# Kernel optimization log

Measured on AMD Instinct MI355X. Metric: run time of the kernel, lower is better.

## Reference

```python
import jax, jax.numpy as jnp
import numpy as np

HIDDEN_DIM = 1024
NUM_HEADS = 16
HEAD_DIM = HIDDEN_DIM // NUM_HEADS


def setup_inputs() -> dict:
    key = jax.random.key(0)
    ks = jax.random.split(key, 9)
    s = 1.0 / np.sqrt(HIDDEN_DIM)
    x = jax.random.normal(ks[0], (2, 2048, HIDDEN_DIM), dtype=jnp.float32)
    Wq = jax.random.uniform(ks[1], (HIDDEN_DIM, HIDDEN_DIM), jnp.float32, -s, s)
    bq = jax.random.uniform(ks[2], (HIDDEN_DIM,), jnp.float32, -s, s)
    Wk = jax.random.uniform(ks[3], (HIDDEN_DIM, HIDDEN_DIM), jnp.float32, -s, s)
    bk = jax.random.uniform(ks[4], (HIDDEN_DIM,), jnp.float32, -s, s)
    Wv = jax.random.uniform(ks[5], (HIDDEN_DIM, HIDDEN_DIM), jnp.float32, -s, s)
    bv = jax.random.uniform(ks[6], (HIDDEN_DIM,), jnp.float32, -s, s)
    Wo = jax.random.uniform(ks[7], (HIDDEN_DIM, HIDDEN_DIM), jnp.float32, -s, s)
    bo = jax.random.uniform(ks[8], (HIDDEN_DIM,), jnp.float32, -s, s)
    return {"x": x, "Wq": Wq, "bq": bq, "Wk": Wk, "bk": bk,
            "Wv": Wv, "bv": bv, "Wo": Wo, "bo": bo}


def reference(x, Wq, bq, Wk, bk, Wv, bv, Wo, bo):
    B, M, D = x.shape
    H, Dh = NUM_HEADS, HEAD_DIM
    # projections -> [B, H, M, Dh]
    def split_heads(t):
        return t.reshape(B, M, H, Dh).transpose(0, 2, 1, 3)
    q = split_heads(x @ Wq.T + bq)
    k = split_heads(x @ Wk.T + bk)
    v = split_heads(x @ Wv.T + bv)
    scores = jnp.einsum('bhmd,bhnd->bhmn', q, k) / np.sqrt(Dh).astype(np.float32)
    # multiplicative diagonal-zero mask: zero the diagonal of the score matrix
    diag_zero = 1.0 - jnp.eye(M, dtype=scores.dtype)  # [M, M]
    scores = scores * diag_zero
    attn = jax.nn.softmax(scores, axis=-1)
    context = jnp.einsum('bhmn,bhnd->bhmd', attn, v)
    context = context.transpose(0, 2, 1, 3).reshape(B, M, D)
    return context @ Wo.T + bo
```

## Files before the change

### kernel.cpp

```cpp
#include <hip/hip_runtime.h>
#include <stdint.h>

typedef _Float16 f16;
typedef __attribute__((ext_vector_type(8))) _Float16 f16x8;
typedef __attribute__((ext_vector_type(4))) _Float16 f16x4;
typedef __attribute__((ext_vector_type(2))) __fp16 fp16x2;
typedef __attribute__((ext_vector_type(4))) float f32x4;

#define HD 1024
#define NH 16
#define DH 64
#define BB 2
#define MM 2048
#define BH (BB*NH)
#define MT (BB*MM)

__device__ __forceinline__ void gl_lds16(const f16* g, f16* l) {
    __builtin_amdgcn_global_load_lds((const __attribute__((address_space(1))) uint32_t*)g,
                                     (__attribute__((address_space(3))) uint32_t*)l, 16, 0, 0);
}

__device__ __forceinline__ float fexp2(float x) {
    float r; asm("v_exp_f32 %0, %1" : "=v"(r) : "v"(x)); return r;
}

__global__ void cvt_all(const float* __restrict__ x,  const float* __restrict__ wq,
                        const float* __restrict__ wk, const float* __restrict__ wv,
                        const float* __restrict__ wo, f16* __restrict__ dst) {
    const int XN4 = MT * HD / 4;
    const int WN4 = HD * HD / 4;
    int i = blockIdx.x * blockDim.x + threadIdx.x;
    if (i >= XN4 + 4 * WN4) return;
    const float* s; int off;
    if (i < XN4) { s = x; off = i; }
    else {
        int k = i - XN4, wsel = k >> 18;
        off = k & (WN4 - 1);
        s = wsel == 0 ? wq : wsel == 1 ? wk : wsel == 2 ? wv : wo;
    }
    float4 v = ((const float4*)s)[off];
    f16x4 h;
    h[0] = (f16)v.x; h[1] = (f16)v.y; h[2] = (f16)v.z; h[3] = (f16)v.w;
    ((f16x4*)dst)[i] = h;
}

template<int MODE>
__global__ __launch_bounds__(256, 3) void gemm_m97(const f16* __restrict__ A,
                                                   const f16* __restrict__ W,
                                                   const float* __restrict__ b0,
                                                   const float* __restrict__ b1,
                                                   const float* __restrict__ b2,
                                                   f16* __restrict__ oh,
                                                   float* __restrict__ of) {
    __shared__ f16 As[128 * 32];
    __shared__ f16 Bs[128 * 32];
    const int bid = blockIdx.x;
    int bn, bm;
    if (MODE == 0) { int xcd = bid & 7, r = bid >> 3; bn = xcd * 3 + (r >> 5); bm = r & 31; }
    else           { bn = bid & 7; bm = bid >> 3; }
    const int t = threadIdx.x, w = t >> 6, lane = t & 63;
    const int wr = w >> 1, wc = w & 1, lr = lane & 15, lg = lane >> 4;
    f32x4 acc[4][4] = {};

    const int srow = w * 16 + (lane >> 2);
    const int schunk = lane & 3;
    const f16* Ab = A + (size_t)(bm * 128) * HD;
    const f16* Wb = W + (size_t)(bn * 128) * HD;
    f16* Asw = As + w * 512;
    f16* Bsw = Bs + w * 512;

    #pragma unroll
    for (int i = 0; i < 2; i++) {
        int r = i * 64 + srow;
        int gc = ((schunk ^ ((r >> 1) & 3)) * 8);
        gl_lds16(Ab + (size_t)r * HD + gc, Asw + i * 2048);
        gl_lds16(Wb + (size_t)r * HD + gc, Bsw + i * 2048);
    }

    for (int k0 = 0;;) {
        __syncthreads();
        f16x8 af[4], bf[4];
        #pragma unroll
        for (int i = 0; i < 4; i++) {
            int ra = wr * 64 + i * 16 + lr;
            af[i] = *(const f16x8*)(As + ra * 32 + ((lg ^ ((ra >> 1) & 3)) * 8));
            int rb = wc * 64 + i * 16 + lr;
            bf[i] = *(const f16x8*)(Bs + rb * 32 + ((lg ^ ((rb >> 1) & 3)) * 8));
        }
        #pragma unroll
        for (int i = 0; i < 4; i++)
            #pragma unroll
            for (int j = 0; j < 4; j++)
                acc[i][j] = __builtin_amdgcn_mfma_f32_16x16x32_f16(af[i], bf[j], acc[i][j], 0, 0, 0);
        k0 += 32;
        if (k0 >= HD) break;
        __syncthreads();
        #pragma unroll
        for (int i = 0; i < 2; i++) {
            int r = i * 64 + srow;
            int gc = ((schunk ^ ((r >> 1) & 3)) * 8);
            gl_lds16(Ab + (size_t)r * HD + k0 + gc, Asw + i * 2048);
            gl_lds16(Wb + (size_t)r * HD + k0 + gc, Bsw + i * 2048);
        }
    }

    if (MODE == 0) {
        const int mat = bn >> 3;
        const float* bp = mat == 0 ? b0 : mat == 1 ? b1 : b2;
        f16* base = oh + (size_t)mat * BH * MM * DH;
        #pragma unroll
        for (int i = 0; i < 4; i++) {
            #pragma unroll
            for (int j = 0; j < 4; j++) {
                int n = bn * 128 + wc * 64 + j * 16 + lr;
                int nn = n & 1023, h = nn >> 6, dh = nn & 63;
                float bvv = bp[nn];
                int mg0 = bm * 128 + wr * 64 + i * 16 + lg * 4;
                int b = mg0 >> 11, mmr0 = mg0 & 2047;
                if (mat == 2) {
                    f16x4 o;
                    #pragma unroll
                    for (int r = 0; r < 4; r++) o[r] = (f16)(acc[i][j][r] + bvv);
                    *(f16x4*)(base + ((size_t)((b * NH + h) * DH + dh)) * MM + mmr0) = o;
                } else {
                    float sc = (mat == 0) ? 0.1803368801111204f : 1.0f;
                    #pragma unroll
                    for (int r = 0; r < 4; r++)
                        base[((size_t)((b * NH + h) * MM + mmr0 + r)) * DH + dh] =
                            (f16)((acc[i][j][r] + bvv) * sc);
                }
            }
        }
    } else {
        #pragma unroll
        for (int i = 0; i < 4; i++)
            #pragma unroll
            for (int j = 0; j < 4; j++) {
                int n = bn * 128 + wc * 64 + j * 16 + lr;
                float bvv = b0[n];
                #pragma unroll
                for (int r = 0; r < 4; r++) {
                    int mg = bm * 128 + wr * 64 + i * 16 + lg * 4 + r;
                    of[(size_t)mg * HD + n] = acc[i][j][r] + bvv;
                }
            }
    }
}

__global__ __launch_bounds__(512, 4) void attn_kernel(const f16* __restrict__ Q,
                                                      const f16* __restrict__ K,
                                                      const f16* __restrict__ Vt,
                                                      f16* __restrict__ ctx) {
    __shared__ f16 Kl[3][64][64];
    __shared__ f16 Vl[3][64][64];
    __shared__ f16 Pl[8][32][32];
    const int bid = blockIdx.x;
    const int xcd = bid & 7, idx = bid >> 3;
    const int bh = xcd * 4 + (idx >> 4);
    const int qblk2 = idx & 15;

    const int t = threadIdx.x, w = t >> 6, lane = t & 63;
    const int lr = lane & 15, lg = lane >> 4;
    const int wq = w >> 1, wkv = w & 1;
    const int q0B = qblk2 * 128 + wq * 32;
    const int kvb = wkv * 32;
    const int dtile = q0B >> 6;
    const bool dwave = (wkv == (wq & 1));

    const f16* Qb = Q + (size_t)bh * MM * DH;
    const f16* Kb = K + (size_t)bh * MM * DH;
    const f16* Vb = Vt + (size_t)bh * DH * MM;

    const int srowS = lane >> 3;
    const int sxc = ((lane & 7) ^ srowS) * 8;
    const int lds_r = w * 8;

    f16x8 qfr[2][2];
    #pragma unroll
    for (int qf = 0; qf < 2; qf++)
        #pragma unroll
        for (int c = 0; c < 2; c++)
            qfr[qf][c] = *(const f16x8*)(Qb + (size_t)(q0B + qf * 16 + lr) * DH + c * 32 + lg * 8);

    f32x4 po[4][2] = {};
    float lsum0 = 0.f, lsum1 = 0.f;
    const int sw = (lr & 7) * 8;
    const int ko0 = (lg * 8) ^ sw, ko1 = (32 + lg * 8) ^ sw;
    const int vko = (kvb + lg * 8) ^ sw;
    const int ps = (lr >> 1) & 3;
    f16* Pw = &Pl[w][0][0];
    const int pro = lr * 32 + ((lg ^ ps) * 8);

    #pragma unroll
    for (int tt = 0; tt < 2; tt++) {
        int row = lds_r + srowS;
        gl_lds16(Kb + (size_t)(tt * 64 + row) * DH + sxc, &Kl[tt][lds_r][0]);
        gl_lds16(Vb + (size_t)row * MM + tt * 64 + sxc, &Vl[tt][lds_r][0]);
    }

#define ATTN_BODY(CUR, NXT, IT, VMN)                                                         \
    {                                                                                        \
        const int it_ = (IT);                                                                \
        asm volatile("s_waitcnt vmcnt(" #VMN ")" ::: "memory");    \
        __builtin_amdgcn_s_barrier();                                  \
        if (it_ < 30) {        \
            const int jn = (it_ + 2) * 64;                                                   \
            int row = lds_r + srowS;                                                         \
            gl_lds16(Kb + (size_t)(jn + row) * DH + sxc, &Kl[NXT][lds_r][0]);                \
            gl_lds16(Vb + (size_t)row * MM + jn + sxc, &Vl[NXT][lds_r][0]);                  \
        }                                                                                    \
        f32x4 s00 = {}, s01 = {}, s10 = {}, s11 = {};                         \
        __builtin_amdgcn_s_setprio(1);                                                       \
        {                                                                                    \
            const f16* kr0 = &Kl[CUR][kvb + lr][0];                                          \
            f16x8 ka = *(const f16x8*)(kr0 + ko0);                                           \
            f16x8 kb = *(const f16x8*)(kr0 + ko1);                                           \
            s00 = __builtin_amdgcn_mfma_f32_16x16x32_f16(ka, qfr[0][0], s00, 0, 0, 0);       \
            s00 = __builtin_amdgcn_mfma_f32_16x16x32_f16(kb, qfr[0][1], s00, 0, 0, 0);       \
            s01 = __builtin_amdgcn_mfma_f32_16x16x32_f16(ka, qfr[1][0], s01, 0, 0, 0);       \
            s01 = __builtin_amdgcn_mfma_f32_16x16x32_f16(kb, qfr[1][1], s01, 0, 0, 0);       \
            const f16* kr1 = &Kl[CUR][kvb + 16 + lr][0];                                     \
            f16x8 kc = *(const f16x8*)(kr1 + ko0);                                           \
            f16x8 kd = *(const f16x8*)(kr1 + ko1);                                           \
            s10 = __builtin_amdgcn_mfma_f32_16x16x32_f16(kc, qfr[0][0], s10, 0, 0, 0);       \
            s10 = __builtin_amdgcn_mfma_f32_16x16x32_f16(kd, qfr[0][1], s10, 0, 0, 0);       \
            s11 = __builtin_amdgcn_mfma_f32_16x16x32_f16(kc, qfr[1][0], s11, 0, 0, 0);       \
            s11 = __builtin_amdgcn_mfma_f32_16x16x32_f16(kd, qfr[1][1], s11, 0, 0, 0);       \
        }                                                                                    \
        __builtin_amdgcn_s_setprio(0);                                                       \
        if (it_ == dtile && dwave) {         \
            int rr = lr - lg * 4;                                                            \
            if (rr >= 0 && rr < 4) { s00[rr] = 0.f; s11[rr] = 0.f; }                         \
        }                                                                                    \
        _Pragma("unroll")                                                                    \
        for (int u = 0; u < 4; u++) {                                                        \
            const f32x4 sv = (u == 0) ? s00 : (u == 1) ? s01 : (u == 2) ? s10 : s11;         \
            const int fq = u >> 1, qf = u & 1;                                               \
            float p0 = fexp2(sv[0]), p1 = fexp2(sv[1]);                                      \
            float p2 = fexp2(sv[2]), p3 = fexp2(sv[3]);                                      \
            if (qf == 0) lsum0 += (p0 + p1) + (p2 + p3);                                     \
            else         lsum1 += (p0 + p1) + (p2 + p3);                                     \
            fp16x2 lo = __builtin_amdgcn_cvt_pkrtz(p0, p1);                                  \
            fp16x2 hi = __builtin_amdgcn_cvt_pkrtz(p2, p3);                                  \
            uint2 pr; pr.x = __builtin_bit_cast(uint32_t, lo);                               \
            pr.y = __builtin_bit_cast(uint32_t, hi);                                         \
            *(f16x4*)(Pw + (qf * 16 + lr) * 32 +                                             \
                      (((fq * 2 + (lg >> 1)) ^ ps) * 8) + (lg & 1) * 4) =                    \
                __builtin_bit_cast(f16x4, pr);                                               \
        }                                                                                    \
        asm volatile("s_waitcnt lgkmcnt(0)" ::: "memory");      \
        f16x8 pf0 = *(const f16x8*)(Pw + pro);                                               \
        f16x8 pf1 = *(const f16x8*)(Pw + 512 + pro);                                         \
        __builtin_amdgcn_s_setprio(1);                                                       \
        _Pragma("unroll")                                                                    \
        for (int df = 0; df < 4; df++) {                                                     \
            const f16* vr = &Vl[CUR][df * 16 + lr][0];                                       \
            f16x8 va = *(const f16x8*)(vr + vko);                                            \
            po[df][0] = __builtin_amdgcn_mfma_f32_16x16x32_f16(va, pf0, po[df][0], 0, 0, 0); \
            po[df][1] = __builtin_amdgcn_mfma_f32_16x16x32_f16(va, pf1, po[df][1], 0, 0, 0); \
        }                                                                                    \
        __builtin_amdgcn_s_setprio(0);                                                       \
    }

    for (int itp = 0; itp < 10; ++itp) {
        ATTN_BODY(0, 2, 3 * itp,     2)
        ATTN_BODY(1, 0, 3 * itp + 1, 2)
        ATTN_BODY(2, 1, 3 * itp + 2, 2)
    }
    ATTN_BODY(0, 2, 30, 2)
    ATTN_BODY(1, 0, 31, 0)
#undef ATTN_BODY

    lsum0 += __shfl_xor(lsum0, 16); lsum0 += __shfl_xor(lsum0, 32);
    lsum1 += __shfl_xor(lsum1, 16); lsum1 += __shfl_xor(lsum1, 32);
    __syncthreads();
    float* shf0 = (float*)(&Kl[0][0][0]);
    float* shf1 = (float*)(&Vl[0][0][0]);
    float* shl  = (float*)(&Pl[0][0][0]);
    const int xi = wq * 64 + lane;
    if (wkv == 1) {
        float* d0 = shf0 + (size_t)xi * 17;
        float* d1 = shf1 + (size_t)xi * 17;
        #pragma unroll
        for (int df = 0; df < 4; df++) {
            *(f32x4*)(d0 + df * 4) = po[df][0];
            *(f32x4*)(d1 + df * 4) = po[df][1];
        }
        shl[xi * 2]     = lsum0;
        shl[xi * 2 + 1] = lsum1;
    }
    __syncthreads();
    if (wkv == 0) {
        const float* s0 = shf0 + (size_t)xi * 17;
        const float* s1 = shf1 + (size_t)xi * 17;
        const float inv0 = 1.f / (lsum0 + shl[xi * 2]);
        const float inv1 = 1.f / (lsum1 + shl[xi * 2 + 1]);
        const int b = bh >> 4, hh = bh & 15;
        #pragma unroll
        for (int qf = 0; qf < 2; qf++) {
            const float inv = qf ? inv1 : inv0;
            const float* s = qf ? s1 : s0;
            f16* cp = ctx + ((size_t)(b * MM + q0B + qf * 16 + lr)) * HD + hh * DH;
            #pragma unroll
            for (int df = 0; df < 4; df++) {
                f16x4 o;
                #pragma unroll
                for (int r = 0; r < 4; r++)
                    o[r] = (f16)((po[df][qf][r] + s[df * 4 + r]) * inv);
                *(f16x4*)(cp + df * 16 + lg * 4) = o;
            }
        }
    }
}

extern "C" void kernel_launch(void* const* d_in, const int* in_sizes, int n_in,
                              void* d_out, int out_size, void* d_ws, size_t ws_size,
                              hipStream_t stream) {
    const float* x  = (const float*)d_in[0];
    const float* Wq = (const float*)d_in[1];
    const float* bq = (const float*)d_in[2];
    const float* Wk = (const float*)d_in[3];
    const float* bk = (const float*)d_in[4];
    const float* Wv = (const float*)d_in[5];
    const float* bv = (const float*)d_in[6];
    const float* Wo = (const float*)d_in[7];
    const float* bo = (const float*)d_in[8];
    float* out = (float*)d_out;

    f16* xh  = (f16*)d_ws;
    f16* wqh = xh  + (size_t)MT * HD;
    f16* woh = wqh + (size_t)3 * HD * HD;
    f16* Qh  = woh + (size_t)HD * HD;
    f16* ctxh= Qh  + (size_t)3 * BH * MM * DH;

    const int total4 = MT * HD / 4 + HD * HD;
    cvt_all<<<(total4 + 255) / 256, 256, 0, stream>>>(x, Wq, Wk, Wv, Wo, xh);

    gemm_m97<0><<<768, 256, 0, stream>>>(xh, wqh, bq, bk, bv, Qh, nullptr);

    attn_kernel<<<512, 512, 0, stream>>>(Qh, Qh + (size_t)BH * MM * DH,
                                         Qh + (size_t)2 * BH * MM * DH, ctxh);

    gemm_m97<1><<<256, 256, 0, stream>>>(ctxh, woh, bo, nullptr, nullptr, nullptr, out);
}
```

Measured before the change: 115.6 us.

## Triple-buffer GEMM LDS tiles with two-stage-ahead async global loads

Replaces the single-buffer load/compute loop in the projection GEMM with a three-slot LDS ring, issuing global-to-LDS loads two K-steps ahead and waiting with explicit vmcnt counts plus one barrier per step. The goal is to hide global memory latency behind MFMA work and remove one of the two barriers per iteration. LDS use per block triples to 48KB, which may lower occupancy against the launch bound of 3 blocks, and correctness depends on the hand-set vmcnt values.

```diff
diff --git a/kernel.cpp b/kernel.cpp
--- a/kernel.cpp
+++ b/kernel.cpp
@@ -52,8 +52,8 @@
                                                    const float* __restrict__ b2,
                                                    f16* __restrict__ oh,
                                                    float* __restrict__ of) {
-    __shared__ f16 As[128 * 32];
-    __shared__ f16 Bs[128 * 32];
+    __shared__ f16 As[3][128 * 32];
+    __shared__ f16 Bs[3][128 * 32];
     const int bid = blockIdx.x;
     int bn, bm;
     if (MODE == 0) { int xcd = bid & 7, r = bid >> 3; bn = xcd * 3 + (r >> 5); bm = r & 31; }
@@ -66,43 +66,47 @@
     const int schunk = lane & 3;
     const f16* Ab = A + (size_t)(bm * 128) * HD;
     const f16* Wb = W + (size_t)(bn * 128) * HD;
-    f16* Asw = As + w * 512;
-    f16* Bsw = Bs + w * 512;
-
-    #pragma unroll
-    for (int i = 0; i < 2; i++) {
-        int r = i * 64 + srow;
-        int gc = ((schunk ^ ((r >> 1) & 3)) * 8);
-        gl_lds16(Ab + (size_t)r * HD + gc, Asw + i * 2048);
-        gl_lds16(Wb + (size_t)r * HD + gc, Bsw + i * 2048);
-    }
-
-    for (int k0 = 0;;) {
-        __syncthreads();
-        f16x8 af[4], bf[4];
-        #pragma unroll
-        for (int i = 0; i < 4; i++) {
-            int ra = wr * 64 + i * 16 + lr;
-            af[i] = *(const f16x8*)(As + ra * 32 + ((lg ^ ((ra >> 1) & 3)) * 8));
-            int rb = wc * 64 + i * 16 + lr;
-            bf[i] = *(const f16x8*)(Bs + rb * 32 + ((lg ^ ((rb >> 1) & 3)) * 8));
-        }
-        #pragma unroll
-        for (int i = 0; i < 4; i++)
-            #pragma unroll
-            for (int j = 0; j < 4; j++)
-                acc[i][j] = __builtin_amdgcn_mfma_f32_16x16x32_f16(af[i], bf[j], acc[i][j], 0, 0, 0);
-        k0 += 32;
-        if (k0 >= HD) break;
-        __syncthreads();
-        #pragma unroll
-        for (int i = 0; i < 2; i++) {
-            int r = i * 64 + srow;
-            int gc = ((schunk ^ ((r >> 1) & 3)) * 8);
-            gl_lds16(Ab + (size_t)r * HD + k0 + gc, Asw + i * 2048);
-            gl_lds16(Wb + (size_t)r * HD + k0 + gc, Bsw + i * 2048);
-        }
-    }
+
+#define GSTAGE(BUF, K0)                                                         \
+    _Pragma("unroll")                                                           \
+    for (int i = 0; i < 2; i++) {                                               \
+        int r = i * 64 + srow;                                                  \
+        int gc = ((schunk ^ ((r >> 1) & 3)) * 8);                               \
+        gl_lds16(Ab + (size_t)r * HD + (K0) + gc, &As[BUF][w * 512 + i * 2048]);\
+        gl_lds16(Wb + (size_t)r * HD + (K0) + gc, &Bs[BUF][w * 512 + i * 2048]);\
+    }
+
+#define GSTEP(CUR, STG, T, VMN)                                                 \
+    {                                                                           \
+        asm volatile("s_waitcnt vmcnt(" #VMN ")" ::: "memory");                 \
+        __builtin_amdgcn_s_barrier();                                           \
+        if ((T) + 2 < 32) { GSTAGE(STG, ((T) + 2) * 32) }                       \
+        f16x8 af[4], bf[4];                                                     \
+        _Pragma("unroll")                                                       \
+        for (int i = 0; i < 4; i++) {                                           \
+            int ra = wr * 64 + i * 16 + lr;                                     \
+            af[i] = *(const f16x8*)(&As[CUR][ra * 32 + ((lg ^ ((ra >> 1) & 3)) * 8)]); \
+            int rb = wc * 64 + i * 16 + lr;                                     \
+            bf[i] = *(const f16x8*)(&Bs[CUR][rb * 32 + ((lg ^ ((rb >> 1) & 3)) * 8)]); \
+        }                                                                       \
+        _Pragma("unroll")                                                       \
+        for (int i = 0; i < 4; i++)                                             \
+            _Pragma("unroll")                                                   \
+            for (int j = 0; j < 4; j++)                                         \
+                acc[i][j] = __builtin_amdgcn_mfma_f32_16x16x32_f16(af[i], bf[j], acc[i][j], 0, 0, 0); \
+    }
+
+    GSTAGE(0, 0)
+    GSTAGE(1, 32)
+    for (int itp = 0; itp < 10; ++itp) {
+        GSTEP(0, 2, 3 * itp,     4)
+        GSTEP(1, 0, 3 * itp + 1, 4)
+        GSTEP(2, 1, 3 * itp + 2, 4)
+    }
+    GSTEP(0, 2, 30, 4)
+    GSTEP(1, 0, 31, 0)
+#undef GSTAGE
+#undef GSTEP
 
     if (MODE == 0) {
         const int mat = bn >> 3;
```

Result: no change. 117.0 us (+1.2%).

## Software-pipeline attention loop: defer PV MFMA one iteration with double-buffered P

Applied to the files above, without the earlier changes.

Restructures the attention main loop so that each iteration first runs the P·V MFMAs for the previous KV tile, then computes QK^T and the exp for the current tile. P gets a double buffer in LDS, and V loads are staged one tile ahead instead of two. The aim is to remove the lgkmcnt(0) stall between writing P and reading it back, so the LDS round-trip latency overlaps with the next tile's QK MFMAs. It costs twice the LDS for P, which may affect occupancy, and needs an epilogue for the final PV.

```diff
diff --git a/kernel.cpp b/kernel.cpp
--- a/kernel.cpp
+++ b/kernel.cpp
@@ -153,7 +153,7 @@
                                                       f16* __restrict__ ctx) {
     __shared__ f16 Kl[3][64][64];
     __shared__ f16 Vl[3][64][64];
-    __shared__ f16 Pl[8][32][32];
+    __shared__ f16 Pl[8][2][32][32];
     const int bid = blockIdx.x;
     const int xcd = bid & 7, idx = bid >> 3;
     const int bh = xcd * 4 + (idx >> 4);
@@ -188,38 +188,54 @@
     const int ko0 = (lg * 8) ^ sw, ko1 = (32 + lg * 8) ^ sw;
     const int vko = (kvb + lg * 8) ^ sw;
     const int ps = (lr >> 1) & 3;
-    f16* Pw = &Pl[w][0][0];
     const int pro = lr * 32 + ((lg ^ ps) * 8);
 
-    #pragma unroll
-    for (int tt = 0; tt < 2; tt++) {
+    {
         int row = lds_r + srowS;
-        gl_lds16(Kb + (size_t)(tt * 64 + row) * DH + sxc, &Kl[tt][lds_r][0]);
-        gl_lds16(Vb + (size_t)row * MM + tt * 64 + sxc, &Vl[tt][lds_r][0]);
-    }
-
-#define ATTN_BODY(CUR, NXT, IT, VMN)                                                         \
+        gl_lds16(Kb + (size_t)row * DH + sxc, &Kl[0][lds_r][0]);
+        gl_lds16(Kb + (size_t)(64 + row) * DH + sxc, &Kl[1][lds_r][0]);
+        gl_lds16(Vb + (size_t)row * MM + sxc, &Vl[0][lds_r][0]);
+    }
+
+#define ABODY(KC, VP, VS, PW, PR, IT, VMN, DOPV)                                             \
     {                                                                                        \
         const int it_ = (IT);                                                                \
-        asm volatile("s_waitcnt vmcnt(" #VMN ")" ::: "memory");    \
-        __builtin_amdgcn_s_barrier();                                  \
-        if (it_ < 30) {        \
-            const int jn = (it_ + 2) * 64;                                                   \
+        asm volatile("s_waitcnt vmcnt(" #VMN ")" ::: "memory");      \
+        __builtin_amdgcn_s_barrier();                                                        \
+        if (it_ + 2 <= 31) {                                                                 \
             int row = lds_r + srowS;                                                         \
-            gl_lds16(Kb + (size_t)(jn + row) * DH + sxc, &Kl[NXT][lds_r][0]);                \
-            gl_lds16(Vb + (size_t)row * MM + jn + sxc, &Vl[NXT][lds_r][0]);                  \
+            gl_lds16(Kb + (size_t)((it_ + 2) * 64 + row) * DH + sxc,                         \
+                     &Kl[(KC + 2) % 3][lds_r][0]);                                           \
+        }                                                                                    \
+        if (it_ + 1 <= 31) {                                                                 \
+            int row = lds_r + srowS;                                                         \
+            gl_lds16(Vb + (size_t)row * MM + (it_ + 1) * 64 + sxc, &Vl[VS][lds_r][0]);       \
+        }                                                                                    \
+        if (DOPV) {        \
+            const f16* Pr = &Pl[w][PR][0][0];                                                \
+            f16x8 pf0 = *(const f16x8*)(Pr + pro);                                           \
+            f16x8 pf1 = *(const f16x8*)(Pr + 512 + pro);                                     \
+            __builtin_amdgcn_s_setprio(1);                                                   \
+            _Pragma("unroll")                                                                \
+            for (int df = 0; df < 4; df++) {                                                 \
+                const f16* vr = &Vl[VP][df * 16 + lr][0];                                    \
+                f16x8 va = *(const f16x8*)(vr + vko);                                        \
+                po[df][0] = __builtin_amdgcn_mfma_f32_16x16x32_f16(va, pf0, po[df][0], 0, 0, 0); \
+                po[df][1] = __builtin_amdgcn_mfma_f32_16x16x32_f16(va, pf1, po[df][1], 0, 0, 0); \
+            }                                                                                \
+            __builtin_amdgcn_s_setprio(0);                                                   \
         }                                                                                    \
         f32x4 s00 = {}, s01 = {}, s10 = {}, s11 = {};                         \
         __builtin_amdgcn_s_setprio(1);                                                       \
         {                                                                                    \
-            const f16* kr0 = &Kl[CUR][kvb + lr][0];                                          \
+            const f16* kr0 = &Kl[KC][kvb + lr][0];                                           \
             f16x8 ka = *(const f16x8*)(kr0 + ko0);                                           \
             f16x8 kb = *(const f16x8*)(kr0 + ko1);                                           \
             s00 = __builtin_amdgcn_mfma_f32_16x16x32_f16(ka, qfr[0][0], s00, 0, 0, 0);       \
             s00 = __builtin_amdgcn_mfma_f32_16x16x32_f16(kb, qfr[0][1], s00, 0, 0, 0);       \
             s01 = __builtin_amdgcn_mfma_f32_16x16x32_f16(ka, qfr[1][0], s01, 0, 0, 0);       \
             s01 = __builtin_amdgcn_mfma_f32_16x16x32_f16(kb, qfr[1][1], s01, 0, 0, 0);       \
-            const f16* kr1 = &Kl[CUR][kvb + 16 + lr][0];                                     \
+            const f16* kr1 = &Kl[KC][kvb + 16 + lr][0];                                      \
             f16x8 kc = *(const f16x8*)(kr1 + ko0);                                           \
             f16x8 kd = *(const f16x8*)(kr1 + ko1);                                           \
             s10 = __builtin_amdgcn_mfma_f32_16x16x32_f16(kc, qfr[0][0], s10, 0, 0, 0);       \
@@ -232,6 +248,7 @@
             int rr = lr - lg * 4;                                                            \
             if (rr >= 0 && rr < 4) { s00[rr] = 0.f; s11[rr] = 0.f; }                         \
         }                                                                                    \
+        f16* Pwr = &Pl[w][PW][0][0];                                                         \
         _Pragma("unroll")                                                                    \
         for (int u = 0; u < 4; u++) {                                                        \
             const f32x4 sv = (u == 0) ? s00 : (u == 1) ? s01 : (u == 2) ? s10 : s11;         \
@@ -244,39 +261,46 @@
             fp16x2 hi = __builtin_amdgcn_cvt_pkrtz(p2, p3);                                  \
             uint2 pr; pr.x = __builtin_bit_cast(uint32_t, lo);                               \
             pr.y = __builtin_bit_cast(uint32_t, hi);                                         \
-            *(f16x4*)(Pw + (qf * 16 + lr) * 32 +                                             \
+            *(f16x4*)(Pwr + (qf * 16 + lr) * 32 +                                            \
                       (((fq * 2 + (lg >> 1)) ^ ps) * 8) + (lg & 1) * 4) =                    \
                 __builtin_bit_cast(f16x4, pr);                                               \
         }                                                                                    \
-        asm volatile("s_waitcnt lgkmcnt(0)" ::: "memory");      \
-        f16x8 pf0 = *(const f16x8*)(Pw + pro);                                               \
-        f16x8 pf1 = *(const f16x8*)(Pw + 512 + pro);                                         \
-        __builtin_amdgcn_s_setprio(1);                                                       \
-        _Pragma("unroll")                                                                    \
-        for (int df = 0; df < 4; df++) {                                                     \
-            const f16* vr = &Vl[CUR][df * 16 + lr][0];                                       \
-            f16x8 va = *(const f16x8*)(vr + vko);                                            \
-            po[df][0] = __builtin_amdgcn_mfma_f32_16x16x32_f16(va, pf0, po[df][0], 0, 0, 0); \
-            po[df][1] = __builtin_amdgcn_mfma_f32_16x16x32_f16(va, pf1, po[df][1], 0, 0, 0); \
-        }                                                                                    \
-        __builtin_amdgcn_s_setprio(0);                                                       \
-    }
-
-    for (int itp = 0; itp < 10; ++itp) {
-        ATTN_BODY(0, 2, 3 * itp,     2)
-        ATTN_BODY(1, 0, 3 * itp + 1, 2)
-        ATTN_BODY(2, 1, 3 * itp + 2, 2)
-    }
-    ATTN_BODY(0, 2, 30, 2)
-    ATTN_BODY(1, 0, 31, 0)
-#undef ATTN_BODY
+    }
+
+    ABODY(0, 2, 1, 0, 1, 0, 2, 0)
+    for (int itp = 0; itp < 5; ++itp) {
+        const int s0 = 6 * itp;
+        ABODY(1, 0, 2, 1, 0, s0 + 1, 2, 1)
+        ABODY(2, 1, 0, 0, 1, s0 + 2, 2, 1)
+        ABODY(0, 2, 1, 1, 0, s0 + 3, 2, 1)
+        ABODY(1, 0, 2, 0, 1, s0 + 4, 2, 1)
+        ABODY(2, 1, 0, 1, 0, s0 + 5, 2, 1)
+        ABODY(0, 2, 1, 0, 1, s0 + 6, 2, 1)
+    }
+    ABODY(1, 0, 2, 1, 0, 31, 1, 1)
+#undef ABODY
+
+    asm volatile("s_waitcnt vmcnt(0)" ::: "memory");
+    __builtin_amdgcn_s_barrier();
+    {
+        const f16* Pr = &Pl[w][1][0][0];
+        f16x8 pf0 = *(const f16x8*)(Pr + pro);
+        f16x8 pf1 = *(const f16x8*)(Pr + 512 + pro);
+        #pragma unroll
+        for (int df = 0; df < 4; df++) {
+            const f16* vr = &Vl[1][df * 16 + lr][0];
+            f16x8 va = *(const f16x8*)(vr + vko);
+            po[df][0] = __builtin_amdgcn_mfma_f32_16x16x32_f16(va, pf0, po[df][0], 0, 0, 0);
+            po[df][1] = __builtin_amdgcn_mfma_f32_16x16x32_f16(va, pf1, po[df][1], 0, 0, 0);
+        }
+    }
 
     lsum0 += __shfl_xor(lsum0, 16); lsum0 += __shfl_xor(lsum0, 32);
     lsum1 += __shfl_xor(lsum1, 16); lsum1 += __shfl_xor(lsum1, 32);
     __syncthreads();
     float* shf0 = (float*)(&Kl[0][0][0]);
     float* shf1 = (float*)(&Vl[0][0][0]);
-    float* shl  = (float*)(&Pl[0][0][0]);
+    float* shl  = (float*)(&Pl[0][0][0][0]);
     const int xi = wq * 64 + lane;
     if (wkv == 1) {
         float* d0 = shf0 + (size_t)xi * 17;
```

Result: slower. 218.4 us (+88.9%).
